# Performance work log

Hardware: AMD Instinct MI355X
Metric: run time of the kernel (lower is better)

## Reference

```python
import jax, jax.numpy as jnp
import numpy as np

EPS = 1e-08
MAX_DELTA_LOG = 0.3
N = 1_000_000
DEG = 4
E = N * DEG
H = 64


def setup_inputs() -> dict:
    key = jax.random.key(0)
    k1, k2, k3, k4, k5, k6 = jax.random.split(key, 6)
    hu_scalar = jax.random.normal(k1, (N,), dtype=jnp.float32) * 50.0 + 100.0
    neighbor_indices = jax.random.randint(k2, (E,), 0, N, dtype=jnp.int64)
    neighbor_offsets = (jnp.arange(N + 1, dtype=jnp.int64) * DEG)  # fixed degree-4 CSR
    W_nei1 = jax.random.normal(k3, (1, H), dtype=jnp.float32) * 0.01
    W_self1 = jax.random.normal(k4, (1, H), dtype=jnp.float32) * 0.01
    b1 = jnp.zeros((H,), dtype=jnp.float32)
    W_nei2 = jax.random.normal(k5, (H,), dtype=jnp.float32) * 0.01
    W_self2 = jax.random.normal(k6, (H,), dtype=jnp.float32) * 0.01
    b2 = jnp.zeros((1,), dtype=jnp.float32)
    return {
        'hu_scalar': hu_scalar,
        'neighbor_indices': neighbor_indices,
        'neighbor_offsets': neighbor_offsets,
        'W_nei1': W_nei1,
        'W_self1': W_self1,
        'b1': b1,
        'W_nei2': W_nei2,
        'W_self2': W_self2,
        'b2': b2,
    }


def reference(hu_scalar, neighbor_indices, neighbor_offsets, W_nei1, W_self1, b1, W_nei2, W_self2, b2):
    n = neighbor_offsets.shape[0] - 1
    e = neighbor_indices.shape[0]
    counts = neighbor_offsets[1:] - neighbor_offsets[:-1]
    # CSR row ids for each edge: repeat_interleave(arange(N), counts)
    row_ids = jnp.repeat(jnp.arange(n, dtype=jnp.int64), counts, total_repeat_length=e)

    h = hu_scalar.astype(jnp.float32)
    mu = h.mean()
    sigma = h.std(ddof=1) + EPS  # torch.std is unbiased
    h0 = (h - mu) / sigma  # (N,)

    # layer 1: scatter-sum of scalar neighbor features
    nei_sum0 = jax.ops.segment_sum(h0[neighbor_indices], row_ids, num_segments=n)  # (N,)
    h1 = jax.nn.relu(b1 + nei_sum0[:, None] * W_nei1 + h0[:, None] * W_self1)  # (N, H)

    # layer 2: scatter-sum of (N,H) features
    nei_sum1 = jax.ops.segment_sum(h1[neighbor_indices], row_ids, num_segments=n)  # (N, H)
    delta_raw = b2 + nei_sum1 @ W_nei2 + h1 @ W_self2  # (N,)
    return MAX_DELTA_LOG * jnp.tanh(delta_raw)
```

## Files before the change

### kernel.cpp

```cpp
#include <hip/hip_runtime.h>
#include <math.h>

#define RED_BLOCKS 1024
#define BLK 256
#define HDIM 64

typedef int   v4i __attribute__((ext_vector_type(4)));
typedef float v4f __attribute__((ext_vector_type(4)));

__global__ void __launch_bounds__(BLK) k_reduce_partial(const float* __restrict__ hu, int n,
                                                        double* __restrict__ part) {
  __shared__ double ls[BLK];
  __shared__ double lq[BLK];
  const v4f* hu4 = (const v4f*)hu;
  const int n4 = n >> 2;
  double s = 0.0, q = 0.0;
  for (int i = blockIdx.x * BLK + threadIdx.x; i < n4; i += RED_BLOCKS * BLK) {
    v4f v = hu4[i];
    double a = (double)v.x, b = (double)v.y, c = (double)v.z, d = (double)v.w;
    s += a + b + c + d;
    q += a * a + b * b + c * c + d * d;
  }
  if (blockIdx.x == 0 && threadIdx.x == 0) {
    for (int i = n4 << 2; i < n; ++i) {
      double v = (double)hu[i];
      s += v;
      q += v * v;
    }
  }
  ls[threadIdx.x] = s;
  lq[threadIdx.x] = q;
  __syncthreads();
  for (int off = BLK / 2; off > 0; off >>= 1) {
    if (threadIdx.x < off) {
      ls[threadIdx.x] += ls[threadIdx.x + off];
      lq[threadIdx.x] += lq[threadIdx.x + off];
    }
    __syncthreads();
  }
  if (threadIdx.x == 0) {
    part[blockIdx.x] = ls[0];
    part[RED_BLOCKS + blockIdx.x] = lq[0];
  }
}

__global__ void __launch_bounds__(BLK) k_reduce_final(const double* __restrict__ part, int n,
                                                      float* __restrict__ stats) {
  __shared__ double ls[BLK];
  __shared__ double lq[BLK];
  double s = 0.0, q = 0.0;
  for (int i = threadIdx.x; i < RED_BLOCKS; i += BLK) {
    s += part[i];
    q += part[RED_BLOCKS + i];
  }
  ls[threadIdx.x] = s;
  lq[threadIdx.x] = q;
  __syncthreads();
  for (int off = BLK / 2; off > 0; off >>= 1) {
    if (threadIdx.x < off) {
      ls[threadIdx.x] += ls[threadIdx.x + off];
      lq[threadIdx.x] += lq[threadIdx.x + off];
    }
    __syncthreads();
  }
  if (threadIdx.x == 0) {
    double sum = ls[0], sumsq = lq[0];
    double mu = sum / (double)n;
    double var = (sumsq - sum * sum / (double)n) / (double)(n - 1);
    if (var < 0.0) var = 0.0;
    double sigma = sqrt(var) + 1e-8;
    stats[0] = (float)mu;
    stats[1] = (float)(1.0 / sigma);
  }
}

__global__ void __launch_bounds__(BLK) k_layer1(
    const float* __restrict__ hu,
    const int* __restrict__ nbr,
    const float* __restrict__ Wn1,
    const float* __restrict__ Ws1,
    const float* __restrict__ B1,
    const float* __restrict__ Wn2,
    const float* __restrict__ Ws2,
    const float* __restrict__ stats,
    float* __restrict__ snei,
    float* __restrict__ sself,
    int n) {
  __shared__ v4f wn1v[HDIM / 4], ws1v[HDIM / 4], bb1v[HDIM / 4], wn2v[HDIM / 4], ws2v[HDIM / 4];
  int t = threadIdx.x;
  if (t < HDIM) {
    ((float*)wn1v)[t] = Wn1[t];
    ((float*)ws1v)[t] = Ws1[t];
    ((float*)bb1v)[t] = B1[t];
    ((float*)wn2v)[t] = Wn2[t];
    ((float*)ws2v)[t] = Ws2[t];
  }
  __syncthreads();
  int u = blockIdx.x * BLK + threadIdx.x;
  if (u >= n) return;
  const float mu = stats[0];
  const float inv = stats[1];
  v4i nb = __builtin_nontemporal_load((const v4i*)nbr + u);
  float hsum = hu[nb.x] + hu[nb.y] + hu[nb.z] + hu[nb.w];
  float a = (hsum - 4.0f * mu) * inv;
  float c = (hu[u] - mu) * inv;
  v4f av = {a, a, a, a};
  v4f cv = {c, c, c, c};
  v4f z = {0.0f, 0.0f, 0.0f, 0.0f};
  v4f sn4 = z, ss4 = z;
#pragma unroll
  for (int j = 0; j < HDIM / 4; ++j) {
    v4f tt = av * wn1v[j] + cv * ws1v[j] + bb1v[j];
    v4f r = __builtin_elementwise_max(tt, z);
    sn4 += r * wn2v[j];
    ss4 += r * ws2v[j];
  }
  float sn = (sn4.x + sn4.y) + (sn4.z + sn4.w);
  float ss = (ss4.x + ss4.y) + (ss4.z + ss4.w);
  __builtin_nontemporal_store(sn, snei + u);
  __builtin_nontemporal_store(ss, sself + u);
}

__global__ void __launch_bounds__(BLK) k_layer2(
    const int* __restrict__ nbr,
    const float* __restrict__ snei,
    const float* __restrict__ sself,
    const float* __restrict__ B2,
    float* __restrict__ out,
    int n) {
  int u = blockIdx.x * BLK + threadIdx.x;
  if (u >= n) return;
  v4i nb = __builtin_nontemporal_load((const v4i*)nbr + u);
  float s = snei[nb.x] + snei[nb.y] + snei[nb.z] + snei[nb.w];
  float ss = __builtin_nontemporal_load(sself + u);
  float d = B2[0] + s + ss;
  __builtin_nontemporal_store(0.3f * tanhf(d), out + u);
}

extern "C" void kernel_launch(void* const* d_in, const int* in_sizes, int n_in,
                              void* d_out, int out_size, void* d_ws, size_t ws_size,
                              hipStream_t stream) {
  const float* hu  = (const float*)d_in[0];
  const int*   nbr = (const int*)d_in[1];
  const float* Wn1 = (const float*)d_in[3];
  const float* Ws1 = (const float*)d_in[4];
  const float* B1  = (const float*)d_in[5];
  const float* Wn2 = (const float*)d_in[6];
  const float* Ws2 = (const float*)d_in[7];
  const float* B2  = (const float*)d_in[8];
  float* out = (float*)d_out;
  const int n = in_sizes[0];

  char* ws = (char*)d_ws;
  double* part = (double*)ws;
  float* stats = (float*)(ws + 2 * RED_BLOCKS * 8);
  float* snei  = (float*)(ws + 32768);
  float* sself = snei + n;

  k_reduce_partial<<<RED_BLOCKS, BLK, 0, stream>>>(hu, n, part);
  k_reduce_final<<<1, BLK, 0, stream>>>(part, n, stats);

  int blocks = (n + BLK - 1) / BLK;
  k_layer1<<<blocks, BLK, 0, stream>>>(hu, nbr, Wn1, Ws1, B1, Wn2, Ws2, stats,
                                       snei, sself, n);
  k_layer2<<<blocks, BLK, 0, stream>>>(nbr, snei, sself, B2, out, n);
}
```

Before: 63.66 us.

## Fuse both GNN layers into one kernel by recomputing neighbor layer-1 outputs

```diff
diff --git a/kernel.cpp b/kernel.cpp
--- a/kernel.cpp
+++ b/kernel.cpp
@@ -1,7 +1,7 @@
 #include <hip/hip_runtime.h>
 #include <math.h>
 
-#define RED_BLOCKS 1024
+#define RED_BLOCKS 256
 #define BLK 256
 #define HDIM 64
 
@@ -44,37 +44,7 @@
   }
 }
 
-__global__ void __launch_bounds__(BLK) k_reduce_final(const double* __restrict__ part, int n,
-                                                      float* __restrict__ stats) {
-  __shared__ double ls[BLK];
-  __shared__ double lq[BLK];
-  double s = 0.0, q = 0.0;
-  for (int i = threadIdx.x; i < RED_BLOCKS; i += BLK) {
-    s += part[i];
-    q += part[RED_BLOCKS + i];
-  }
-  ls[threadIdx.x] = s;
-  lq[threadIdx.x] = q;
-  __syncthreads();
-  for (int off = BLK / 2; off > 0; off >>= 1) {
-    if (threadIdx.x < off) {
-      ls[threadIdx.x] += ls[threadIdx.x + off];
-      lq[threadIdx.x] += lq[threadIdx.x + off];
-    }
-    __syncthreads();
-  }
-  if (threadIdx.x == 0) {
-    double sum = ls[0], sumsq = lq[0];
-    double mu = sum / (double)n;
-    double var = (sumsq - sum * sum / (double)n) / (double)(n - 1);
-    if (var < 0.0) var = 0.0;
-    double sigma = sqrt(var) + 1e-8;
-    stats[0] = (float)mu;
-    stats[1] = (float)(1.0 / sigma);
-  }
-}
-
-__global__ void __launch_bounds__(BLK) k_layer1(
+__global__ void __launch_bounds__(BLK) k_main(
     const float* __restrict__ hu,
     const int* __restrict__ nbr,
     const float* __restrict__ Wn1,
@@ -82,58 +52,86 @@
     const float* __restrict__ B1,
     const float* __restrict__ Wn2,
     const float* __restrict__ Ws2,
-    const float* __restrict__ stats,
-    float* __restrict__ snei,
-    float* __restrict__ sself,
+    const float* __restrict__ B2,
+    const double* __restrict__ part,
+    float* __restrict__ out,
     int n) {
-  __shared__ v4f wn1v[HDIM / 4], ws1v[HDIM / 4], bb1v[HDIM / 4], wn2v[HDIM / 4], ws2v[HDIM / 4];
-  int t = threadIdx.x;
+  __shared__ v4f w4[HDIM];
+  __shared__ float bb[HDIM];
+  __shared__ double red_s[BLK];
+  __shared__ double red_q[BLK];
+  __shared__ float sstat[2];
+
+  const int t = threadIdx.x;
+  red_s[t] = part[t];
+  red_q[t] = part[RED_BLOCKS + t];
   if (t < HDIM) {
-    ((float*)wn1v)[t] = Wn1[t];
-    ((float*)ws1v)[t] = Ws1[t];
-    ((float*)bb1v)[t] = B1[t];
-    ((float*)wn2v)[t] = Wn2[t];
-    ((float*)ws2v)[t] = Ws2[t];
+    v4f w;
+    w.x = Wn1[t];
+    w.y = Ws1[t];
+    w.z = Wn2[t];
+    w.w = Ws2[t];
+    w4[t] = w;
+    bb[t] = B1[t];
   }
   __syncthreads();
-  int u = blockIdx.x * BLK + threadIdx.x;
+  for (int off = BLK / 2; off > 0; off >>= 1) {
+    if (t < off) {
+      red_s[t] += red_s[t + off];
+      red_q[t] += red_q[t + off];
+    }
+    __syncthreads();
+  }
+  if (t == 0) {
+    double sum = red_s[0], sumsq = red_q[0];
+    double mu = sum / (double)n;
+    double var = (sumsq - sum * sum / (double)n) / (double)(n - 1);
+    if (var < 0.0) var = 0.0;
+    double sigma = sqrt(var) + 1e-8;
+    sstat[0] = (float)mu;
+    sstat[1] = (float)(1.0 / sigma);
+  }
+  __syncthreads();
+
+  const int u = blockIdx.x * BLK + t;
   if (u >= n) return;
-  const float mu = stats[0];
-  const float inv = stats[1];
-  v4i nb = __builtin_nontemporal_load((const v4i*)nbr + u);
-  float hsum = hu[nb.x] + hu[nb.y] + hu[nb.z] + hu[nb.w];
-  float a = (hsum - 4.0f * mu) * inv;
-  float c = (hu[u] - mu) * inv;
-  v4f av = {a, a, a, a};
-  v4f cv = {c, c, c, c};
+  const float mu = sstat[0];
+  const float inv = sstat[1];
+  const v4i* nbr4 = (const v4i*)nbr;
+
+  v4i nb = nbr4[u];
+  float h0v = hu[nb.x], h1v = hu[nb.y], h2v = hu[nb.z], h3v = hu[nb.w];
+  float h_u = hu[u];
+  v4i nb0 = nbr4[nb.x];
+  v4i nb1 = nbr4[nb.y];
+  v4i nb2 = nbr4[nb.z];
+  v4i nb3 = nbr4[nb.w];
+  v4f hs;
+  hs.x = (hu[nb0.x] + hu[nb0.y]) + (hu[nb0.z] + hu[nb0.w]);
+  hs.y = (hu[nb1.x] + hu[nb1.y]) + (hu[nb1.z] + hu[nb1.w]);
+  hs.z = (hu[nb2.x] + hu[nb2.y]) + (hu[nb2.z] + hu[nb2.w]);
+  hs.w = (hu[nb3.x] + hu[nb3.y]) + (hu[nb3.z] + hu[nb3.w]);
+
+  v4f hn = {h0v, h1v, h2v, h3v};
+  v4f a4 = (hs - 4.0f * mu) * inv;
+  v4f c4 = (hn - mu) * inv;
+  float a_u = (((h0v + h1v) + (h2v + h3v)) - 4.0f * mu) * inv;
+  float c_u = (h_u - mu) * inv;
+
   v4f z = {0.0f, 0.0f, 0.0f, 0.0f};
-  v4f sn4 = z, ss4 = z;
+  v4f sn4 = z;
+  float ss = 0.0f;
 #pragma unroll
-  for (int j = 0; j < HDIM / 4; ++j) {
-    v4f tt = av * wn1v[j] + cv * ws1v[j] + bb1v[j];
+  for (int j = 0; j < HDIM; ++j) {
+    v4f w = w4[j];
+    float bj = bb[j];
+    v4f tt = a4 * w.x + c4 * w.y + bj;
     v4f r = __builtin_elementwise_max(tt, z);
-    sn4 += r * wn2v[j];
-    ss4 += r * ws2v[j];
+    sn4 += r * w.z;
+    float ts = fmaf(a_u, w.x, fmaf(c_u, w.y, bj));
+    ss = fmaf(fmaxf(ts, 0.0f), w.w, ss);
   }
-  float sn = (sn4.x + sn4.y) + (sn4.z + sn4.w);
-  float ss = (ss4.x + ss4.y) + (ss4.z + ss4.w);
-  __builtin_nontemporal_store(sn, snei + u);
-  __builtin_nontemporal_store(ss, sself + u);
-}
-
-__global__ void __launch_bounds__(BLK) k_layer2(
-    const int* __restrict__ nbr,
-    const float* __restrict__ snei,
-    const float* __restrict__ sself,
-    const float* __restrict__ B2,
-    float* __restrict__ out,
-    int n) {
-  int u = blockIdx.x * BLK + threadIdx.x;
-  if (u >= n) return;
-  v4i nb = __builtin_nontemporal_load((const v4i*)nbr + u);
-  float s = snei[nb.x] + snei[nb.y] + snei[nb.z] + snei[nb.w];
-  float ss = __builtin_nontemporal_load(sself + u);
-  float d = B2[0] + s + ss;
+  float d = B2[0] + ((sn4.x + sn4.y) + (sn4.z + sn4.w)) + ss;
   __builtin_nontemporal_store(0.3f * tanhf(d), out + u);
 }
 
@@ -151,17 +149,10 @@
   float* out = (float*)d_out;
   const int n = in_sizes[0];
 
-  char* ws = (char*)d_ws;
-  double* part = (double*)ws;
-  float* stats = (float*)(ws + 2 * RED_BLOCKS * 8);
-  float* snei  = (float*)(ws + 32768);
-  float* sself = snei + n;
+  double* part = (double*)d_ws;
 
   k_reduce_partial<<<RED_BLOCKS, BLK, 0, stream>>>(hu, n, part);
-  k_reduce_final<<<1, BLK, 0, stream>>>(part, n, stats);
-
   int blocks = (n + BLK - 1) / BLK;
-  k_layer1<<<blocks, BLK, 0, stream>>>(hu, nbr, Wn1, Ws1, B1, Wn2, Ws2, stats,
-                                       snei, sself, n);
-  k_layer2<<<blocks, BLK, 0, stream>>>(nbr, snei, sself, B2, out, n);
+  k_main<<<blocks, BLK, 0, stream>>>(hu, nbr, Wn1, Ws1, B1, Wn2, Ws2, B2,
+                                     part, out, n);
 }
```

Measured after the change: 169.6 us. 166% more time.
